# Performance work log

Hardware: AMD Instinct MI355X
Metric: run time of the kernel (lower is better)

The kernel has to match this reference:

```python
import jax, jax.numpy as jnp
import numpy as np

N = 10000
E = 160000
IN_DIM = 256
PROJ_DIM = 512
HIDDEN = 512
OUT_DIM = 512
HEADS1, HEADS2, HEADS3 = 4, 4, 1
NEG_SLOPE = 0.2  # PyG GATConv default


def gat_conv(x, edge_index, W, att_src, att_dst, bias, heads, out_c, concat):
    """PyG GATConv (eval mode), with self-loops already appended to edge_index.
    x: [N, F_in]; W: [F_in, heads*out_c]; att_src/att_dst: [heads, out_c]; bias: [heads*out_c] or [out_c]."""
    n = x.shape[0]
    h = (x @ W).reshape(n, heads, out_c)            # [N, H, C]
    a_src = jnp.einsum('nhc,hc->nh', h, att_src)     # [N, H]
    a_dst = jnp.einsum('nhc,hc->nh', h, att_dst)     # [N, H]
    src, dst = edge_index[0], edge_index[1]
    e = jax.nn.leaky_relu(a_src[src] + a_dst[dst], NEG_SLOPE)  # [E, H]
    # segment softmax over incoming edges per destination node
    e_max = jax.ops.segment_max(e, dst, num_segments=n)
    e_exp = jnp.exp(e - e_max[dst])
    denom = jax.ops.segment_sum(e_exp, dst, num_segments=n)
    alpha = e_exp / denom[dst]                       # [E, H]
    msg = alpha[:, :, None] * h[src]                 # [E, H, C]
    out = jax.ops.segment_sum(msg, dst, num_segments=n)  # [N, H, C]
    out = out.reshape(n, heads * out_c) if concat else out.mean(axis=1)
    return out + bias


def setup_inputs() -> dict:
    key = jax.random.key(0)
    ks = jax.random.split(key, 16)
    g = 0.1
    inp = {
        'x': jax.random.normal(ks[0], (N, IN_DIM), dtype=jnp.float32),
        'edge_index': jax.random.randint(ks[1], (2, E), 0, N, dtype=jnp.int64),
        'proj_W': jax.random.normal(ks[2], (IN_DIM, PROJ_DIM), dtype=jnp.float32) * g,
        'proj_b': jnp.zeros((PROJ_DIM,), dtype=jnp.float32),
        'W1': jax.random.normal(ks[3], (PROJ_DIM, HEADS1 * HIDDEN), dtype=jnp.float32) * g,
        'as1': jax.random.normal(ks[4], (HEADS1, HIDDEN), dtype=jnp.float32) * g,
        'ad1': jax.random.normal(ks[5], (HEADS1, HIDDEN), dtype=jnp.float32) * g,
        'b1': jnp.zeros((HEADS1 * HIDDEN,), dtype=jnp.float32),
        'W2': jax.random.normal(ks[6], (HEADS1 * HIDDEN, HEADS2 * HIDDEN), dtype=jnp.float32) * g * 0.5,
        'as2': jax.random.normal(ks[7], (HEADS2, HIDDEN), dtype=jnp.float32) * g,
        'ad2': jax.random.normal(ks[8], (HEADS2, HIDDEN), dtype=jnp.float32) * g,
        'b2': jnp.zeros((HEADS2 * HIDDEN,), dtype=jnp.float32),
        'W3': jax.random.normal(ks[9], (HEADS2 * HIDDEN, HEADS3 * OUT_DIM), dtype=jnp.float32) * g * 0.5,
        'as3': jax.random.normal(ks[10], (HEADS3, OUT_DIM), dtype=jnp.float32) * g,
        'ad3': jax.random.normal(ks[11], (HEADS3, OUT_DIM), dtype=jnp.float32) * g,
        'b3': jnp.zeros((OUT_DIM,), dtype=jnp.float32),
    }
    return inp


def reference(x, edge_index, proj_W, proj_b, W1, as1, ad1, b1, W2, as2, ad2, b2, W3, as3, ad3, b3):
    # append self-loops once (PyG GATConv add_self_loops=True)
    loops = jnp.arange(N, dtype=edge_index.dtype)
    ei = jnp.concatenate([edge_index, jnp.stack([loops, loops])], axis=1)
    h = x @ proj_W + proj_b                                   # [N, 512]
    h = jax.nn.elu(gat_conv(h, ei, W1, as1, ad1, b1, HEADS1, HIDDEN, True))
    h = jax.nn.elu(gat_conv(h, ei, W2, as2, ad2, b2, HEADS2, HIDDEN, True))
    return gat_conv(h, ei, W3, as3, ad3, b3, HEADS3, OUT_DIM, False)  # [N, 512]
```

## Files before the change

### kernel.cpp

```cpp
#include <hip/hip_runtime.h>
#include <hip/hip_bf16.h>


#define LB(x) __launch_bounds__(x)

typedef unsigned short u16;
typedef unsigned int u32;
typedef __attribute__((ext_vector_type(8))) short short8;
typedef __attribute__((ext_vector_type(8))) short bf16x8;
typedef __attribute__((ext_vector_type(8))) _Float16 f16x8;
typedef __attribute__((ext_vector_type(4))) float f32x4;

__device__ __forceinline__ float b2f(u16 u) {
    union { float f; u32 u; } x;
    x.u = ((u32)u) << 16;
    return x.f;
}
__device__ __forceinline__ u16 f2b(float f) {
    u32 u = __float_as_uint(f);
    u = (u + 0x7FFFu + ((u >> 16) & 1u)) >> 16;
    return (u16)u;
}
__device__ __forceinline__ u16 f2h(float f) {
    union { _Float16 h; u16 u; } x;
    x.h = (_Float16)f;
    return x.u;
}
__device__ __forceinline__ float h2f(u16 u) {
    union { _Float16 h; u16 u; } x;
    x.u = u;
    return (float)x.h;
}
__device__ __forceinline__ void lds_cp16(const void* g, void* l) {
    __builtin_amdgcn_global_load_lds(
        (const __attribute__((address_space(1))) unsigned int*)g,
        (__attribute__((address_space(3))) unsigned int*)l, 16, 0, 0);
}

__global__ void k_deg(const int* __restrict__ ei, int E, int Np, int* __restrict__ deg) {
    int e = blockIdx.x * blockDim.x + threadIdx.x;
    if (e >= E + Np) return;
    int dst = (e < E) ? ei[E + e] : (e - E);
    atomicAdd(&deg[dst], 1);
}

__global__ LB(256) void k_s1(const int* __restrict__ deg, int* __restrict__ row_ptr,
                             int* __restrict__ bsum, int n) {
    __shared__ int sh[256];
    int b = blockIdx.x, t = threadIdx.x;
    int i = b * 256 + t;
    int v = (i < n) ? deg[i] : 0;
    sh[t] = v;
    __syncthreads();
    #pragma unroll
    for (int off = 1; off < 256; off <<= 1) {
        int add = (t >= off) ? sh[t - off] : 0;
        __syncthreads();
        sh[t] += add;
        __syncthreads();
    }
    if (i < n) row_ptr[i + 1] = sh[t];
    if (t == 255) bsum[b] = sh[255];
}

__global__ LB(64) void k_s2(int* __restrict__ bsum, int* __restrict__ boff, int nb) {
    __shared__ int sh[64];
    int t = threadIdx.x;
    sh[t] = (t < nb) ? bsum[t] : 0;
    __syncthreads();
    #pragma unroll
    for (int off = 1; off < 64; off <<= 1) {
        int add = (t >= off) ? sh[t - off] : 0;
        __syncthreads();
        sh[t] += add;
        __syncthreads();
    }
    if (t < nb) boff[t] = (t == 0) ? 0 : sh[t - 1];
}

__global__ LB(256) void k_s3(const int* __restrict__ deg, int* __restrict__ row_ptr,
                             const int* __restrict__ boff, int* __restrict__ cursor, int n) {
    int b = blockIdx.x, t = threadIdx.x;
    int i = b * 256 + t;
    if (i == 0) row_ptr[0] = 0;
    if (i < n) {
        int inc = row_ptr[i + 1] + boff[b];
        row_ptr[i + 1] = inc;
        cursor[i] = inc - deg[i];
    }
}

__global__ void k_fill(const int* __restrict__ ei, int E, int Np,
                       int* __restrict__ cursor, int* __restrict__ col_src) {
    int e = blockIdx.x * blockDim.x + threadIdx.x;
    if (e >= E + Np) return;
    int src, dst;
    if (e < E) { src = ei[e]; dst = ei[E + e]; }
    else       { src = dst = e - E; }
    int pos = atomicAdd(&cursor[dst], 1);
    col_src[pos] = src;
}

__global__ void k_pack(const float* __restrict__ in, u16* __restrict__ hi,
                       u16* __restrict__ lo, int n4) {
    int i = blockIdx.x * blockDim.x + threadIdx.x;
    if (i >= n4) return;
    float4 v = ((const float4*)in)[i];
    ushort4 h, l;
    h.x = f2b(v.x); l.x = f2b(v.x - b2f(h.x));
    h.y = f2b(v.y); l.y = f2b(v.y - b2f(h.y));
    h.z = f2b(v.z); l.z = f2b(v.z - b2f(h.z));
    h.w = f2b(v.w); l.w = f2b(v.w - b2f(h.w));
    ((ushort4*)hi)[i] = h;
    ((ushort4*)lo)[i] = l;
}

template<bool F16S>
__global__ LB(256) void k_wt_pack(const float* __restrict__ W, u16* __restrict__ Whi,
                                  u16* __restrict__ Wlo, int K, int Nn) {
    __shared__ float sh[32][33];
    int n0 = blockIdx.x * 32, k0 = blockIdx.y * 32;
    int c = threadIdx.x & 31, r0 = threadIdx.x >> 5;
    #pragma unroll
    for (int r = r0; r < 32; r += 8)
        sh[r][c] = W[(size_t)(k0 + r) * Nn + n0 + c];
    __syncthreads();
    #pragma unroll
    for (int r = r0; r < 32; r += 8) {
        float v = sh[c][r];
        if (F16S) {
            Whi[(size_t)(n0 + r) * K + k0 + c] = f2h(v);
        } else {
            u16 hi = f2b(v);
            Whi[(size_t)(n0 + r) * K + k0 + c] = hi;
            Wlo[(size_t)(n0 + r) * K + k0 + c] = f2b(v - b2f(hi));
        }
    }
}

__global__ LB(64) void k_bfold(const float* __restrict__ pb,
                               const u16* __restrict__ w1t_hi, const u16* __restrict__ w1t_lo,
                               float* __restrict__ bfold, int K) {
    int n = blockIdx.x;
    int lane = threadIdx.x;
    float s = 0.f;
    for (int k = lane; k < K; k += 64) {
        float w = b2f(w1t_hi[(size_t)n * K + k]) + b2f(w1t_lo[(size_t)n * K + k]);
        s = fmaf(pb[k], w, s);
    }
    #pragma unroll
    for (int off = 32; off; off >>= 1) s += __shfl_xor(s, off);
    if (lane == 0) bfold[n] = s;
}

template<int WM, int NFR, int PREC, int OUTMODE, bool ATT, bool DB>
__global__ __launch_bounds__(WM * 128)
void k_gemm_pl(const u16* __restrict__ Ahi, const u16* __restrict__ Alo,
               const u16* __restrict__ Bhi, const u16* __restrict__ Blo,
               const float* __restrict__ bias,
               u16* __restrict__ Chi, u16* __restrict__ Clo,
               u16* __restrict__ Cf16,
               const float* __restrict__ att_s, const float* __restrict__ att_d,
               float* __restrict__ a_src, float* __restrict__ a_dst,
               int HH, int M, int K, int Nn) {
    constexpr int BM = WM * 64;
    constexpr int BN = NFR * 32;
    constexpr int T  = WM * 128;
    constexpr int BITER = ((NFR * 128) / T > 0) ? (NFR * 128) / T : 1;
    constexpr int NBUF = DB ? 2 : 1;
    constexpr int ASZ = BM * 32;
    constexpr int BSZ = BN * 32;
    __shared__ u16 AsHi[NBUF * ASZ];
    __shared__ u16 AsLo[(PREC == 0) ? NBUF * ASZ : 8];
    __shared__ u16 BsHi[NBUF * BSZ];
    __shared__ u16 BsLo[(PREC == 0) ? NBUF * BSZ : 8];
    const int tid  = threadIdx.x;
    const int lane = tid & 63;
    const int w    = tid >> 6;
    const int wr   = w >> 1;
    const int wc   = w & 1;
    const int row0 = blockIdx.y * BM;
    const int col0 = blockIdx.x * BN;
    const int ln15 = lane & 15;
    const int lq   = lane >> 4;

    f32x4 acc[4][NFR];
    #pragma unroll
    for (int m = 0; m < 4; ++m)
        #pragma unroll
        for (int n = 0; n < NFR; ++n) acc[m][n] = (f32x4){0.f, 0.f, 0.f, 0.f};

    auto STAGE = [&](int k0, int buf) {
        size_t ab = (size_t)buf * ASZ * 2;
        size_t bb = (size_t)buf * BSZ * 2;
        #pragma unroll
        for (int i = 0; i < 2; ++i) {
            int c = i * T + tid;
            int r  = 2 * (c >> 3) + (((c >> 2) ^ (c >> 4)) & 1);
            int kc = (c & 3) ^ (r & 3);
            int gra = row0 + r; if (gra >= M) gra = M - 1;
            size_t ga = (size_t)gra * K + k0 + kc * 8;
            lds_cp16(Ahi + ga, (char*)AsHi + ab + c * 16);
            if (PREC == 0) lds_cp16(Alo + ga, (char*)AsLo + ab + c * 16);
        }
        #pragma unroll
        for (int i = 0; i < BITER; ++i) {
            int c = i * T + tid;
            int r  = 2 * (c >> 3) + (((c >> 2) ^ (c >> 4)) & 1);
            int kc = (c & 3) ^ (r & 3);
            size_t gb = (size_t)(col0 + r) * K + k0 + kc * 8;
            lds_cp16(Bhi + gb, (char*)BsHi + bb + c * 16);
            if (PREC == 0) lds_cp16(Blo + gb, (char*)BsLo + bb + c * 16);
        }
    };

    auto COMPUTE = [&](int buf) {
        size_t ab = (size_t)buf * ASZ * 2;
        size_t bb = (size_t)buf * BSZ * 2;
        if (PREC == 0) {
            bf16x8 ah[4], al[4], bh[NFR], bl[NFR];
            #pragma unroll
            for (int m = 0; m < 4; ++m) {
                int row = wr * 64 + m * 16 + ln15;
                size_t byo = (size_t)((row * 64 + lq * 16) ^ ((row & 7) << 4));
                ah[m] = *(const bf16x8*)((const char*)AsHi + ab + byo);
                al[m] = *(const bf16x8*)((const char*)AsLo + ab + byo);
            }
            #pragma unroll
            for (int n = 0; n < NFR; ++n) {
                int row = wc * (NFR * 16) + n * 16 + ln15;
                size_t byo = (size_t)((row * 64 + lq * 16) ^ ((row & 7) << 4));
                bh[n] = *(const bf16x8*)((const char*)BsHi + bb + byo);
                bl[n] = *(const bf16x8*)((const char*)BsLo + bb + byo);
            }
            #pragma unroll
            for (int m = 0; m < 4; ++m)
                #pragma unroll
                for (int n = 0; n < NFR; ++n) {
                    acc[m][n] = __builtin_amdgcn_mfma_f32_16x16x32_bf16(al[m], bh[n], acc[m][n], 0, 0, 0);
                    acc[m][n] = __builtin_amdgcn_mfma_f32_16x16x32_bf16(ah[m], bl[n], acc[m][n], 0, 0, 0);
                    acc[m][n] = __builtin_amdgcn_mfma_f32_16x16x32_bf16(ah[m], bh[n], acc[m][n], 0, 0, 0);
                }
        } else {
            f16x8 a[4], b[NFR];
            #pragma unroll
            for (int m = 0; m < 4; ++m) {
                int row = wr * 64 + m * 16 + ln15;
                size_t byo = (size_t)((row * 64 + lq * 16) ^ ((row & 7) << 4));
                a[m] = *(const f16x8*)((const char*)AsHi + ab + byo);
            }
            #pragma unroll
            for (int n = 0; n < NFR; ++n) {
                int row = wc * (NFR * 16) + n * 16 + ln15;
                size_t byo = (size_t)((row * 64 + lq * 16) ^ ((row & 7) << 4));
                b[n] = *(const f16x8*)((const char*)BsHi + bb + byo);
            }
            #pragma unroll
            for (int m = 0; m < 4; ++m)
                #pragma unroll
                for (int n = 0; n < NFR; ++n)
                    acc[m][n] = __builtin_amdgcn_mfma_f32_16x16x32_f16(a[m], b[n], acc[m][n], 0, 0, 0);
        }
    };

    if (DB) {
        const int nt = K >> 5;
        STAGE(0, 0);
        __syncthreads();
        for (int t = 0; t < nt; ++t) {
            int cur = t & 1;
            if (t + 1 < nt) STAGE((t + 1) << 5, cur ^ 1);
            COMPUTE(cur);
            __syncthreads();
        }
    } else {
        for (int k0 = 0; k0 < K; k0 += 32) {
            STAGE(k0, 0);
            __syncthreads();
            COMPUTE(0);
            __syncthreads();
        }
    }

    #pragma unroll
    for (int m = 0; m < 4; ++m) {
        #pragma unroll
        for (int n = 0; n < NFR; ++n) {
            int gc = col0 + wc * (NFR * 16) + n * 16 + ln15;
            float badd = bias ? bias[gc] : 0.f;
            #pragma unroll
            for (int j = 0; j < 4; ++j) {
                int gr = row0 + wr * 64 + m * 16 + lq * 4 + j;
                if (gr < M) {
                    float v = acc[m][n][j] + badd;
                    size_t o = (size_t)gr * Nn + gc;
                    if (OUTMODE == 0) {
                        u16 hi = f2b(v);
                        Chi[o] = hi;
                        Clo[o] = f2b(v - b2f(hi));
                    } else {
                        Cf16[o] = f2h(v);
                    }
                }
            }
        }
    }

    if (ATT) {
        float atts[NFR], attd[NFR], bb[NFR];
        #pragma unroll
        for (int n = 0; n < NFR; ++n) {
            int gc = col0 + wc * (NFR * 16) + n * 16 + ln15;
            atts[n] = att_s[gc];
            attd[n] = att_d[gc];
            bb[n]   = bias ? bias[gc] : 0.f;
        }
        const int head = (col0 + wc * (NFR * 16)) >> 9;
        #pragma unroll
        for (int m = 0; m < 4; ++m) {
            #pragma unroll
            for (int j = 0; j < 4; ++j) {
                int gr = row0 + wr * 64 + m * 16 + lq * 4 + j;
                float s1 = 0.f, s2 = 0.f;
                #pragma unroll
                for (int n = 0; n < NFR; ++n) {
                    float v = acc[m][n][j] + bb[n];
                    s1 = fmaf(v, atts[n], s1);
                    s2 = fmaf(v, attd[n], s2);
                }
                #pragma unroll
                for (int off = 1; off < 16; off <<= 1) {
                    s1 += __shfl_xor(s1, off);
                    s2 += __shfl_xor(s2, off);
                }
                if (ln15 == 0 && gr < M) {
                    atomicAdd(&a_src[gr * HH + head], s1);
                    atomicAdd(&a_dst[gr * HH + head], s2);
                }
            }
        }
    }
}

template <int HH, int OMODE, bool ELU_>
__global__ __launch_bounds__(HH * 64)
void k_sagg(const int* __restrict__ row_ptr, const int* __restrict__ col_src,
            const float* __restrict__ a_src, const float* __restrict__ a_dst,
            const u16* __restrict__ hf, const float* __restrict__ bias,
            u16* __restrict__ Oh, float* __restrict__ Of, int C) {
    __shared__ float sal[HH * 64];
    const int d    = blockIdx.x;
    const int tid  = threadIdx.x;
    const int w    = tid >> 6;
    const int lane = tid & 63;
    const int F    = HH * C;
    const int o    = tid * 8;
    const int s = row_ptr[d], eend = row_ptr[d + 1];
    const int cnt = eend - s;
    const float adh = a_dst[d * HH + w];

    float acc[8];
    #pragma unroll
    for (int j = 0; j < 8; ++j) acc[j] = 0.f;

    if (cnt <= 64) {
        bool act = lane < cnt;
        float av = act ? a_src[col_src[s + lane] * HH + w] : 0.f;
        float x = av + adh;
        x = (x > 0.f) ? x : 0.2f * x;
        float v = act ? x : -1e30f;
        float m = v;
        #pragma unroll
        for (int off = 32; off; off >>= 1) m = fmaxf(m, __shfl_xor(m, off));
        float e_ = act ? __expf(v - m) : 0.f;
        float sum = e_;
        #pragma unroll
        for (int off = 32; off; off >>= 1) sum += __shfl_xor(sum, off);
        if (act) sal[w * 64 + lane] = e_ / sum;
        __syncthreads();

        short8 v0, v1; float a0, a1;
        if (cnt > 0) { v0 = *(const short8*)(hf + (size_t)col_src[s] * F + o); a0 = sal[w * 64]; }
        if (cnt > 1) { v1 = *(const short8*)(hf + (size_t)col_src[s + 1] * F + o); a1 = sal[w * 64 + 1]; }
        int i = 0;
        for (; i + 2 <= cnt; i += 2) {
            short8 t0, t1; float b0, b1;
            bool m0 = (i + 2 < cnt), m1 = (i + 3 < cnt);
            if (m0) { t0 = *(const short8*)(hf + (size_t)col_src[s + i + 2] * F + o); b0 = sal[w * 64 + i + 2]; }
            if (m1) { t1 = *(const short8*)(hf + (size_t)col_src[s + i + 3] * F + o); b1 = sal[w * 64 + i + 3]; }
            #pragma unroll
            for (int j = 0; j < 8; ++j) acc[j] = fmaf(a0, h2f((u16)v0[j]), acc[j]);
            #pragma unroll
            for (int j = 0; j < 8; ++j) acc[j] = fmaf(a1, h2f((u16)v1[j]), acc[j]);
            if (m0) { v0 = t0; a0 = b0; }
            if (m1) { v1 = t1; a1 = b1; }
        }
        if (i < cnt) {
            #pragma unroll
            for (int j = 0; j < 8; ++j) acc[j] = fmaf(a0, h2f((u16)v0[j]), acc[j]);
        }
    } else {
        float m = -1e30f;
        for (int e = s + lane; e < eend; e += 64) {
            float x = a_src[col_src[e] * HH + w] + adh;
            x = (x > 0.f) ? x : 0.2f * x;
            m = fmaxf(m, x);
        }
        #pragma unroll
        for (int off = 32; off; off >>= 1) m = fmaxf(m, __shfl_xor(m, off));
        float sum = 0.f;
        for (int e = s + lane; e < eend; e += 64) {
            float x = a_src[col_src[e] * HH + w] + adh;
            x = (x > 0.f) ? x : 0.2f * x;
            sum += __expf(x - m);
        }
        #pragma unroll
        for (int off = 32; off; off >>= 1) sum += __shfl_xor(sum, off);
        float inv = 1.0f / sum;
        for (int base = s; base < eend; base += 64) {
            int e = base + lane;
            if (e < eend) {
                float x = a_src[col_src[e] * HH + w] + adh;
                x = (x > 0.f) ? x : 0.2f * x;
                sal[w * 64 + lane] = __expf(x - m) * inv;
            }
            __syncthreads();
            int nn = (eend - base < 64) ? (eend - base) : 64;
            for (int i = 0; i < nn; ++i) {
                int src = col_src[base + i];
                float a = sal[w * 64 + i];
                short8 vv = *(const short8*)(hf + (size_t)src * F + o);
                #pragma unroll
                for (int j = 0; j < 8; ++j)
                    acc[j] = fmaf(a, h2f((u16)vv[j]), acc[j]);
            }
            __syncthreads();
        }
    }

    #pragma unroll
    for (int j = 0; j < 8; ++j) {
        acc[j] += bias[o + j];
        if (ELU_) acc[j] = (acc[j] > 0.f) ? acc[j] : __expf(acc[j]) - 1.f;
    }
    if (OMODE == 0) {
        short8 r;
        #pragma unroll
        for (int j = 0; j < 8; ++j) r[j] = (short)f2h(acc[j]);
        *(short8*)(Oh + (size_t)d * F + o) = r;
    } else {
        float* po = Of + (size_t)d * F + o;
        #pragma unroll
        for (int j4 = 0; j4 < 2; ++j4) {
            float4 r;
            r.x = acc[j4 * 4 + 0]; r.y = acc[j4 * 4 + 1];
            r.z = acc[j4 * 4 + 2]; r.w = acc[j4 * 4 + 3];
            *(float4*)&po[j4 * 4] = r;
        }
    }
}

extern "C" void kernel_launch(void* const* d_in, const int* in_sizes, int n_in,
                              void* d_out, int out_size, void* d_ws, size_t ws_size,
                              hipStream_t stream) {
    const float* x      = (const float*)d_in[0];
    const int*   ei     = (const int*)d_in[1];
    const float* proj_W = (const float*)d_in[2];
    const float* proj_b = (const float*)d_in[3];
    const float* W1  = (const float*)d_in[4];
    const float* as1 = (const float*)d_in[5];
    const float* ad1 = (const float*)d_in[6];
    const float* b1  = (const float*)d_in[7];
    const float* W2  = (const float*)d_in[8];
    const float* as2 = (const float*)d_in[9];
    const float* ad2 = (const float*)d_in[10];
    const float* b2  = (const float*)d_in[11];
    const float* W3  = (const float*)d_in[12];
    const float* as3 = (const float*)d_in[13];
    const float* ad3 = (const float*)d_in[14];
    const float* b3  = (const float*)d_in[15];

    const int N  = in_sizes[0] / 256;
    const int E  = in_sizes[1] / 2;
    const int Ep = E + N;
    const int NB = (N + 255) / 256;

    size_t off = 0;
    auto alloc = [&](size_t bytes) -> void* {
        void* p = (char*)d_ws + off;
        off += (bytes + 255) & ~(size_t)255;
        return p;
    };
    u16* bufX    = (u16*)alloc((size_t)N * 2048 * 2);
    u16* bufY    = (u16*)alloc((size_t)N * 2048 * 2);
    u16* xb_hi   = (u16*)alloc((size_t)N * 256 * 2);
    u16* xb_lo   = (u16*)alloc((size_t)N * 256 * 2);
    u16* pw_hi   = (u16*)alloc((size_t)256 * 512 * 2);
    u16* pw_lo   = (u16*)alloc((size_t)256 * 512 * 2);
    u16* wf_hi   = (u16*)alloc((size_t)2048 * 256 * 2);
    u16* wf_lo   = (u16*)alloc((size_t)2048 * 256 * 2);
    float* bfold   = (float*)alloc((size_t)2048 * 4);
    float* att_z   = (float*)alloc((size_t)N * 18 * 4);
    int*   deg     = (int*)alloc((size_t)N * 4);
    int*   cursor  = (int*)alloc((size_t)N * 4);
    int*   row_ptr = (int*)alloc((size_t)(N + 1) * 4);
    int*   col_src = (int*)alloc((size_t)Ep * 4);
    int*   bsum    = (int*)alloc((size_t)NB * 4);
    int*   boff    = (int*)alloc((size_t)NB * 4);
    (void)ws_size;

    float* a_src1 = att_z;
    float* a_dst1 = att_z + (size_t)N * 4;
    float* a_src2 = att_z + (size_t)N * 8;
    float* a_dst2 = att_z + (size_t)N * 12;
    float* a_src3 = att_z + (size_t)N * 16;
    float* a_dst3 = att_z + (size_t)N * 17;

    u16* whi = (u16*)d_out;
    u16* wlo = (u16*)d_out + (size_t)2048 * 2048;

    hipMemsetAsync(deg, 0, (size_t)N * 4, stream);
    hipMemsetAsync(att_z, 0, (size_t)N * 18 * 4, stream);
    int eb = (Ep + 255) / 256;
    k_deg<<<eb, 256, 0, stream>>>(ei, E, N, deg);
    k_s1<<<NB, 256, 0, stream>>>(deg, row_ptr, bsum, N);
    k_s2<<<1, 64, 0, stream>>>(bsum, boff, NB);
    k_s3<<<NB, 256, 0, stream>>>(deg, row_ptr, boff, cursor, N);
    k_fill<<<eb, 256, 0, stream>>>(ei, E, N, cursor, col_src);

    const int MB1 = (N + 127) / 128;
    const int MB2 = (N + 255) / 256;

    k_pack<<<(N * 256 / 4 + 255) / 256, 256, 0, stream>>>(x, xb_hi, xb_lo, N * 256 / 4);
    k_pack<<<(256 * 512 / 4 + 255) / 256, 256, 0, stream>>>(proj_W, pw_hi, pw_lo, 256 * 512 / 4);

    k_wt_pack<false><<<dim3(2048 / 32, 512 / 32), 256, 0, stream>>>(W1, whi, wlo, 512, 2048);
    k_bfold<<<2048, 64, 0, stream>>>(proj_b, whi, wlo, bfold, 512);
    k_gemm_pl<2, 2, 0, 0, false, false><<<dim3(256 / 64, 2048 / 128), 256, 0, stream>>>(
        whi, wlo, pw_hi, pw_lo, nullptr, wf_hi, wf_lo, nullptr,
        nullptr, nullptr, nullptr, nullptr, 0, 2048, 512, 256);

    k_gemm_pl<2, 4, 0, 2, true, false><<<dim3(2048 / 128, MB1), 256, 0, stream>>>(
        xb_hi, xb_lo, wf_hi, wf_lo, bfold, nullptr, nullptr, bufX,
        as1, ad1, a_src1, a_dst1, 4, N, 256, 2048);
    k_sagg<4, 0, true><<<N, 256, 0, stream>>>(row_ptr, col_src, a_src1, a_dst1,
                                              bufX, b1, bufY, nullptr, 512);

    k_wt_pack<true><<<dim3(2048 / 32, 2048 / 32), 256, 0, stream>>>(W2, whi, nullptr, 2048, 2048);
    k_gemm_pl<4, 4, 2, 2, true, true><<<dim3(2048 / 128, MB2), 512, 0, stream>>>(
        bufY, nullptr, whi, nullptr, nullptr, nullptr, nullptr, bufX,
        as2, ad2, a_src2, a_dst2, 4, N, 2048, 2048);
    k_sagg<4, 0, true><<<N, 256, 0, stream>>>(row_ptr, col_src, a_src2, a_dst2,
                                              bufX, b2, bufY, nullptr, 512);

    k_wt_pack<true><<<dim3(512 / 32, 2048 / 32), 256, 0, stream>>>(W3, whi, nullptr, 2048, 512);
    k_gemm_pl<2, 2, 2, 2, true, true><<<dim3(512 / 64, MB1), 256, 0, stream>>>(
        bufY, nullptr, whi, nullptr, nullptr, nullptr, nullptr, bufX,
        as3, ad3, a_src3, a_dst3, 1, N, 2048, 512);
    k_sagg<1, 1, false><<<N, 64, 0, stream>>>(row_ptr, col_src, a_src3, a_dst3,
                                              bufX, b3, nullptr, (float*)d_out, 512);
}
```

Baseline: 619.2 us.

## Replace double-buffer syncthreads with prefetch-two pipeline using fine-grained vmcnt waits

In the f16 GEMM kernels for layers 2 and 3, the double-buffered loop now issues the first two k-tile loads up front. Each iteration waits on vmcnt so the next tile's loads stay in flight, and uses raw s_barrier with sched_barrier fences around compute. The buffer just consumed is refilled two tiles ahead, so global-to-LDS copies overlap more of the MFMA work. This depends on the hardcoded vmcnt(3) matching the loads per stage, which a static_assert checks. The PREC==0 lo buffers are also shrunk to a single buffer.

```diff
diff --git a/kernel.cpp b/kernel.cpp
--- a/kernel.cpp
+++ b/kernel.cpp
@@ -153,7 +153,7 @@
     if (lane == 0) bfold[n] = s;
 }
 
-template<int WM, int NFR, int PREC, int OUTMODE, bool ATT, bool DB>
+template<int WM, int NFR, int PREC, int OUTMODE, bool ATT, int PIPE>
 __global__ __launch_bounds__(WM * 128)
 void k_gemm_pl(const u16* __restrict__ Ahi, const u16* __restrict__ Alo,
                const u16* __restrict__ Bhi, const u16* __restrict__ Blo,
@@ -167,13 +167,14 @@
     constexpr int BN = NFR * 32;
     constexpr int T  = WM * 128;
     constexpr int BITER = ((NFR * 128) / T > 0) ? (NFR * 128) / T : 1;
-    constexpr int NBUF = DB ? 2 : 1;
+    constexpr int NBUF = (PIPE == 2) ? 2 : 1;
     constexpr int ASZ = BM * 32;
     constexpr int BSZ = BN * 32;
+    static_assert(PIPE != 2 || (PREC == 2 && 2 + BITER == 3), "PIPE2 needs LPT==3");
     __shared__ u16 AsHi[NBUF * ASZ];
-    __shared__ u16 AsLo[(PREC == 0) ? NBUF * ASZ : 8];
+    __shared__ u16 AsLo[(PREC == 0) ? ASZ : 8];
     __shared__ u16 BsHi[NBUF * BSZ];
-    __shared__ u16 BsLo[(PREC == 0) ? NBUF * BSZ : 8];
+    __shared__ u16 BsLo[(PREC == 0) ? BSZ : 8];
     const int tid  = threadIdx.x;
     const int lane = tid & 63;
     const int w    = tid >> 6;
@@ -201,7 +202,7 @@
             int gra = row0 + r; if (gra >= M) gra = M - 1;
             size_t ga = (size_t)gra * K + k0 + kc * 8;
             lds_cp16(Ahi + ga, (char*)AsHi + ab + c * 16);
-            if (PREC == 0) lds_cp16(Alo + ga, (char*)AsLo + ab + c * 16);
+            if (PREC == 0) lds_cp16(Alo + ga, (char*)AsLo + c * 16);
         }
         #pragma unroll
         for (int i = 0; i < BITER; ++i) {
@@ -210,7 +211,7 @@
             int kc = (c & 3) ^ (r & 3);
             size_t gb = (size_t)(col0 + r) * K + k0 + kc * 8;
             lds_cp16(Bhi + gb, (char*)BsHi + bb + c * 16);
-            if (PREC == 0) lds_cp16(Blo + gb, (char*)BsLo + bb + c * 16);
+            if (PREC == 0) lds_cp16(Blo + gb, (char*)BsLo + c * 16);
         }
     };
 
@@ -224,14 +225,14 @@
                 int row = wr * 64 + m * 16 + ln15;
                 size_t byo = (size_t)((row * 64 + lq * 16) ^ ((row & 7) << 4));
                 ah[m] = *(const bf16x8*)((const char*)AsHi + ab + byo);
-                al[m] = *(const bf16x8*)((const char*)AsLo + ab + byo);
+                al[m] = *(const bf16x8*)((const char*)AsLo + byo);
             }
             #pragma unroll
             for (int n = 0; n < NFR; ++n) {
                 int row = wc * (NFR * 16) + n * 16 + ln15;
                 size_t byo = (size_t)((row * 64 + lq * 16) ^ ((row & 7) << 4));
                 bh[n] = *(const bf16x8*)((const char*)BsHi + bb + byo);
-                bl[n] = *(const bf16x8*)((const char*)BsLo + bb + byo);
+                bl[n] = *(const bf16x8*)((const char*)BsLo + byo);
             }
             #pragma unroll
             for (int m = 0; m < 4; ++m)
@@ -263,15 +264,22 @@
         }
     };
 
-    if (DB) {
+    if (PIPE == 2) {
         const int nt = K >> 5;
         STAGE(0, 0);
-        __syncthreads();
+        if (nt > 1) STAGE(32, 1);
         for (int t = 0; t < nt; ++t) {
-            int cur = t & 1;
-            if (t + 1 < nt) STAGE((t + 1) << 5, cur ^ 1);
-            COMPUTE(cur);
-            __syncthreads();
+            if (t + 1 < nt) {
+                asm volatile("s_waitcnt vmcnt(3)" ::: "memory");
+            } else {
+                asm volatile("s_waitcnt vmcnt(0)" ::: "memory");
+            }
+            __builtin_amdgcn_s_barrier();
+            __builtin_amdgcn_sched_barrier(0);
+            COMPUTE(t & 1);
+            __builtin_amdgcn_sched_barrier(0);
+            __builtin_amdgcn_s_barrier();
+            if (t + 2 < nt) STAGE((t + 2) << 5, t & 1);
         }
     } else {
         for (int k0 = 0; k0 < K; k0 += 32) {
@@ -536,25 +544,25 @@
 
     k_wt_pack<false><<<dim3(2048 / 32, 512 / 32), 256, 0, stream>>>(W1, whi, wlo, 512, 2048);
     k_bfold<<<2048, 64, 0, stream>>>(proj_b, whi, wlo, bfold, 512);
-    k_gemm_pl<2, 2, 0, 0, false, false><<<dim3(256 / 64, 2048 / 128), 256, 0, stream>>>(
+    k_gemm_pl<2, 2, 0, 0, false, 0><<<dim3(256 / 64, 2048 / 128), 256, 0, stream>>>(
         whi, wlo, pw_hi, pw_lo, nullptr, wf_hi, wf_lo, nullptr,
         nullptr, nullptr, nullptr, nullptr, 0, 2048, 512, 256);
 
-    k_gemm_pl<2, 4, 0, 2, true, false><<<dim3(2048 / 128, MB1), 256, 0, stream>>>(
+    k_gemm_pl<2, 4, 0, 2, true, 0><<<dim3(2048 / 128, MB1), 256, 0, stream>>>(
         xb_hi, xb_lo, wf_hi, wf_lo, bfold, nullptr, nullptr, bufX,
         as1, ad1, a_src1, a_dst1, 4, N, 256, 2048);
     k_sagg<4, 0, true><<<N, 256, 0, stream>>>(row_ptr, col_src, a_src1, a_dst1,
                                               bufX, b1, bufY, nullptr, 512);
 
     k_wt_pack<true><<<dim3(2048 / 32, 2048 / 32), 256, 0, stream>>>(W2, whi, nullptr, 2048, 2048);
-    k_gemm_pl<4, 4, 2, 2, true, true><<<dim3(2048 / 128, MB2), 512, 0, stream>>>(
+    k_gemm_pl<4, 4, 2, 2, true, 2><<<dim3(2048 / 128, MB2), 512, 0, stream>>>(
         bufY, nullptr, whi, nullptr, nullptr, nullptr, nullptr, bufX,
         as2, ad2, a_src2, a_dst2, 4, N, 2048, 2048);
     k_sagg<4, 0, true><<<N, 256, 0, stream>>>(row_ptr, col_src, a_src2, a_dst2,
                                               bufX, b2, bufY, nullptr, 512);
 
     k_wt_pack<true><<<dim3(512 / 32, 2048 / 32), 256, 0, stream>>>(W3, whi, nullptr, 2048, 512);
-    k_gemm_pl<2, 2, 2, 2, true, true><<<dim3(512 / 64, MB1), 256, 0, stream>>>(
+    k_gemm_pl<2, 2, 2, 2, true, 2><<<dim3(512 / 64, MB1), 256, 0, stream>>>(
         bufY, nullptr, whi, nullptr, nullptr, nullptr, nullptr, bufX,
         as3, ad3, a_src3, a_dst3, 1, N, 2048, 512);
     k_sagg<1, 1, false><<<N, 64, 0, stream>>>(row_ptr, col_src, a_src3, a_dst3,
```

After: 622.7 us, median of 2. Within noise of the previous version (+0.6%).
